# Optimization experiments

Measured on AMD Instinct MI355X. Metric: run time of the kernel, lower is better.

## Reference

```python
import jax, jax.numpy as jnp
import numpy as np

B, N, A = 8, 256, 180  # batch, resolution (even), n_angles


def setup_inputs() -> dict:
    key = jax.random.key(0)
    imgs = jax.random.normal(jax.random.fold_in(key, 0), (B, N, N), dtype=jnp.float32)
    # uniformly spaced projection angles over [0, pi)
    angles = jnp.linspace(0.0, np.pi, A, endpoint=False).astype(jnp.float32)
    return {"imgs": imgs, "angles": angles}


def _radon_forward(imgs, angles):
    """Parallel-beam Radon forward projection via bilinear ray sampling.

    imgs:   [B, N, N] float image batch
    angles: [A] float projection angles (radians)
    returns sinogram [B, A, N] (detector count == resolution, unit step along ray)
    """
    n = imgs.shape[-1]
    dtype = imgs.dtype
    c = (n - 1) / 2.0  # image center in pixel coords
    s = jnp.arange(n, dtype=dtype) - c  # detector positions, centered
    t = s                                # integration steps along each ray
    cos = jnp.cos(angles)[:, None, None]  # [A,1,1]
    sin = jnp.sin(angles)[:, None, None]
    # Sample point for (angle a, detector s_i, step t_j), in pixel coordinates.
    x = s[None, :, None] * cos - t[None, None, :] * sin + c  # [A, N, N]
    y = s[None, :, None] * sin + t[None, None, :] * cos + c  # [A, N, N]

    x0 = jnp.floor(x)
    y0 = jnp.floor(y)
    wx = x - x0
    wy = y - y0
    x0i = x0.astype(jnp.int32)
    y0i = y0.astype(jnp.int32)

    def corner(xi, yi, w):
        # zero-padding outside the image: mask out-of-range samples
        inb = (xi >= 0) & (xi < n) & (yi >= 0) & (yi < n)
        xc = jnp.clip(xi, 0, n - 1)
        yc = jnp.clip(yi, 0, n - 1)
        vals = imgs[:, yc, xc]  # gather -> [B, A, N, N]
        return vals * (w * inb.astype(dtype))[None]

    acc = (corner(x0i, y0i, (1.0 - wx) * (1.0 - wy))
           + corner(x0i + 1, y0i, wx * (1.0 - wy))
           + corner(x0i, y0i + 1, (1.0 - wx) * wy)
           + corner(x0i + 1, y0i + 1, wx * wy))
    return acc.sum(axis=-1)  # line integral along t -> [B, A, N]


def reference(imgs, angles):
    return _radon_forward(imgs, angles)
```

## Files before the change

kernel.cpp:

```cpp
#include <hip/hip_runtime.h>
#include <hip/hip_fp16.h>

#define NREZ 256
#define NB 8
#define NA 180

#define GW 258
#define GBYTES ((size_t)GW * GW * 16)

#define LWMAX 52
#define LH 47
#define CHUNK_T 32
#define NCHUNK (NREZ / CHUNK_T)

__device__ __forceinline__ __half2 bc_h2(unsigned int v) {
    return __builtin_bit_cast(__half2, v);
}

__device__ __forceinline__ void dma16(const uint4* g, uint4* l) {
    __builtin_amdgcn_global_load_lds(
        (const __attribute__((address_space(1))) void*)g,
        (__attribute__((address_space(3))) void*)l, 16, 0, 0);
}

__global__ __launch_bounds__(256) void build_fp16g(const float* __restrict__ img,
                                                   uint4* __restrict__ gbuf) {
    const int gy = blockIdx.x;
    for (int gx = threadIdx.x; gx < GW; gx += 256) {
        uint4 v = make_uint4(0u, 0u, 0u, 0u);
        const int x = gx - 1, y = gy - 1;
        if (x >= 0 && x < NREZ && y >= 0 && y < NREZ) {
            const int p = (y << 8) + x;
            unsigned short h[NB];
#pragma unroll
            for (int b = 0; b < NB; ++b)
                h[b] = __half_as_ushort(__float2half_rn(img[b * (NREZ * NREZ) + p]));
            v.x = (unsigned)h[0] | ((unsigned)h[1] << 16);
            v.y = (unsigned)h[2] | ((unsigned)h[3] << 16);
            v.z = (unsigned)h[4] | ((unsigned)h[5] << 16);
            v.w = (unsigned)h[6] | ((unsigned)h[7] << 16);
        }
        gbuf[(size_t)gy * GW + gx] = v;
    }
}

__global__ __launch_bounds__(256, 4) void radon_dma(const uint4* __restrict__ gbuf,
                                                    const float* __restrict__ angles,
                                                    float* __restrict__ out) {
    __shared__ uint4 tile[LWMAX * LH];

    const int a = blockIdx.x;
    const int tid = threadIdx.x;
    const int wave = tid >> 6;
    const int lane = tid & 63;
    const int ls = lane & 31;
    const int lp = lane >> 5;
    const int sIdx = blockIdx.y * 32 + ls;
    const int tw = 2 * wave + lp;

    const float C = 127.5f;
    float sn, cs;
    sincosf(angles[a], &sn, &cs);

    int LWr = 47;
    {
        float best = -1.f;
#pragma unroll
        for (int w = 47; w <= LWMAX; ++w) {
            const float sig = fmaf(sn, (float)w, cs);
            const float u = sig - 2.f * floorf(sig * 0.5f);
            const float m = 1.f - fabsf(u - 1.f);
            if (m > best) { best = m; LWr = w; }
        }
    }

    const float s = (float)sIdx - C;
    const float xs = fmaf(s, cs, C);
    const float ys = fmaf(s, sn, C);

    const float s_lo = (float)(blockIdx.y * 32) - C;
    const float s_hi = s_lo + 31.f;
    const float xsl = fmaf(s_lo, cs, C), xsh = fmaf(s_hi, cs, C);
    const float ysl = fmaf(s_lo, sn, C), ysh = fmaf(s_hi, sn, C);

    auto window = [&](int ck, int& bxs, int& bys, bool& interior, bool& empty,
                      int& hh, int& wl) {
        const float t_lo = (float)(ck * CHUNK_T) - C;
        const float t_hi = t_lo + 31.f;
        const float x00 = fmaf(t_lo, -sn, xsl), x01 = fmaf(t_hi, -sn, xsl);
        const float x10 = fmaf(t_lo, -sn, xsh), x11 = fmaf(t_hi, -sn, xsh);
        const float y00 = fmaf(t_lo, cs, ysl), y01 = fmaf(t_hi, cs, ysl);
        const float y10 = fmaf(t_lo, cs, ysh), y11 = fmaf(t_hi, cs, ysh);
        const int bx = (int)floorf(fminf(fminf(x00, x01), fminf(x10, x11)));
        const int by = (int)floorf(fminf(fminf(y00, y01), fminf(y10, y11)));
        const int mx = (int)floorf(fmaxf(fmaxf(x00, x01), fmaxf(x10, x11)));
        const int my = (int)floorf(fmaxf(fmaxf(y00, y01), fmaxf(y10, y11)));
        bxs = min(max(bx, -1), 210);
        bys = min(max(by, -1), 210);
        interior = (bx >= 0) && (by >= 0) && (bx <= 210) && (by <= 210);
        empty = (bx > 255) || (by > 255) || (mx < -1) || (my < -1);
        hh = min(LH, max(my - bys + 2, 0));
        wl = interior ? 46 : 47;
    };

    auto stage = [&](int bxs, int bys, int hh, int wl) {
#pragma unroll
        for (int k = 0; k < 12; ++k) {
            const int row = wave + 4 * k;
            if (row < hh && lane < wl) {
                const uint4* gp = gbuf + (size_t)(bys + row + 1) * GW + (bxs + 1) + lane;
                dma16(gp, &tile[row * LWr]);
            }
        }
    };

    float accf[NB];
#pragma unroll
    for (int b = 0; b < NB; ++b) accf[b] = 0.f;
    const __half2 hz = __float2half2_rn(0.f);

    int bxs, bys, hh, wl;
    bool interior, empty;
    window(0, bxs, bys, interior, empty, hh, wl);
    if (!empty) stage(bxs, bys, hh, wl);

    for (int ck = 0; ck < NCHUNK; ++ck) {
        __syncthreads();

        const float t_lo = (float)(ck * CHUNK_T) - C;
        __half2 acc01 = hz, acc23 = hz, acc45 = hz, acc67 = hz;

        auto samp = [&](float tt, bool chk) {
            const float x = fmaf(tt, -sn, xs);
            const float y = fmaf(tt, cs, ys);
            const float xf = floorf(x), yf = floorf(y);
            const int u0 = (int)xf, v0 = (int)yf;
            if (!chk || (u0 >= -1 && u0 <= 255 && v0 >= -1 && v0 <= 255)) {
                const float wu = x - xf, wv = y - yf;
                const float au = 1.f - wu, av = 1.f - wv;
                const __half2 w00 = __float2half2_rn(au * av);
                const __half2 w10 = __float2half2_rn(wu * av);
                const __half2 w01 = __float2half2_rn(au * wv);
                const __half2 w11 = __float2half2_rn(wu * wv);
                const int dx = u0 - bxs;
                const int r = v0 - bys;
                const int b00 = r * LWr + dx;
                const int b10 = b00 + LWr;
                const uint4 p00 = tile[b00];
                const uint4 p10 = tile[b00 + 1];
                const uint4 p01 = tile[b10];
                const uint4 p11 = tile[b10 + 1];
                acc01 = __hfma2(w00, bc_h2(p00.x), acc01);
                acc01 = __hfma2(w10, bc_h2(p10.x), acc01);
                acc01 = __hfma2(w01, bc_h2(p01.x), acc01);
                acc01 = __hfma2(w11, bc_h2(p11.x), acc01);
                acc23 = __hfma2(w00, bc_h2(p00.y), acc23);
                acc23 = __hfma2(w10, bc_h2(p10.y), acc23);
                acc23 = __hfma2(w01, bc_h2(p01.y), acc23);
                acc23 = __hfma2(w11, bc_h2(p11.y), acc23);
                acc45 = __hfma2(w00, bc_h2(p00.z), acc45);
                acc45 = __hfma2(w10, bc_h2(p10.z), acc45);
                acc45 = __hfma2(w01, bc_h2(p01.z), acc45);
                acc45 = __hfma2(w11, bc_h2(p11.z), acc45);
                acc67 = __hfma2(w00, bc_h2(p00.w), acc67);
                acc67 = __hfma2(w10, bc_h2(p10.w), acc67);
                acc67 = __hfma2(w01, bc_h2(p01.w), acc67);
                acc67 = __hfma2(w11, bc_h2(p11.w), acc67);
            }
        };

        if (!empty) {
            if (interior) {
#pragma unroll
                for (int it = 0; it < 4; ++it)
                    samp(t_lo + (float)(tw + 8 * it), false);
            } else {
#pragma unroll
                for (int it = 0; it < 4; ++it)
                    samp(t_lo + (float)(tw + 8 * it), true);
            }
            accf[0] += __low2float(acc01); accf[1] += __high2float(acc01);
            accf[2] += __low2float(acc23); accf[3] += __high2float(acc23);
            accf[4] += __low2float(acc45); accf[5] += __high2float(acc45);
            accf[6] += __low2float(acc67); accf[7] += __high2float(acc67);
        }

        __syncthreads();

        if (ck + 1 < NCHUNK) {
            window(ck + 1, bxs, bys, interior, empty, hh, wl);
            if (!empty) stage(bxs, bys, hh, wl);
        }
    }

#pragma unroll
    for (int b = 0; b < NB; ++b) accf[b] += __shfl_xor(accf[b], 32);

    float4* red4 = (float4*)tile;
    if (lane < 32) {
        red4[(wave * 32 + lane) * 2 + 0] = make_float4(accf[0], accf[1], accf[2], accf[3]);
        red4[(wave * 32 + lane) * 2 + 1] = make_float4(accf[4], accf[5], accf[6], accf[7]);
    }
    __syncthreads();
    {
        const float* red = (const float*)tile;
        const int b = tid >> 5;
        const int ss = tid & 31;
        const int base = ss * 8 + b;
        const float sum = red[base] + red[256 + base] + red[512 + base] + red[768 + base];
        out[(b * NA + a) * NREZ + blockIdx.y * 32 + ss] = sum;
    }
}

__global__ __launch_bounds__(256) void radon_plain(const float* __restrict__ img,
                                                   const float* __restrict__ angles,
                                                   float* __restrict__ out) {
    const int a = blockIdx.x;
    const int tid = threadIdx.x;
    const int wave = tid >> 6;
    const int lane = tid & 63;
    const int s_sub = lane & 7;
    const int t_sub = lane >> 3;
    const int sIdx = blockIdx.y * 32 + wave * 8 + s_sub;
    const float c = 127.5f;
    float sn, cs;
    sincosf(angles[a], &sn, &cs);
    const float s = (float)sIdx - c;
    float acc[NB];
#pragma unroll
    for (int b = 0; b < NB; ++b) acc[b] = 0.f;
    for (int j = 0; j < NREZ / 8; ++j) {
        const float tt = (float)(t_sub + 8 * j) - c;
        const float x = s * cs - tt * sn + c;
        const float y = s * sn + tt * cs + c;
        const float xf = floorf(x), yf = floorf(y);
        const int u0 = (int)xf, v0 = (int)yf;
        if (u0 < -1 || u0 >= NREZ || v0 < -1 || v0 >= NREZ) continue;
        const float wu = x - xf, wv = y - yf;
        const bool iu0 = (u0 >= 0), iu1 = (u0 + 1 <= NREZ - 1);
        const bool iv0 = (v0 >= 0), iv1 = (v0 + 1 <= NREZ - 1);
        const float w00 = (1.f - wu) * (1.f - wv) * ((iu0 && iv0) ? 1.f : 0.f);
        const float w10 = wu * (1.f - wv) * ((iu1 && iv0) ? 1.f : 0.f);
        const float w01 = (1.f - wu) * wv * ((iu0 && iv1) ? 1.f : 0.f);
        const float w11 = wu * wv * ((iu1 && iv1) ? 1.f : 0.f);
        const int u0c = min(max(u0, 0), NREZ - 1);
        const int u1c = min(u0 + 1, NREZ - 1);
        const int v0c = min(max(v0, 0), NREZ - 1);
        const int v1c = min(v0 + 1, NREZ - 1);
#pragma unroll
        for (int b = 0; b < NB; ++b) {
            const float* p = img + b * (NREZ * NREZ);
            acc[b] += w00 * p[v0c * NREZ + u0c] + w10 * p[v0c * NREZ + u1c] +
                      w01 * p[v1c * NREZ + u0c] + w11 * p[v1c * NREZ + u1c];
        }
    }
#pragma unroll
    for (int b = 0; b < NB; ++b) {
        float v = acc[b];
        v += __shfl_xor(v, 8);
        v += __shfl_xor(v, 16);
        v += __shfl_xor(v, 32);
        acc[b] = v;
    }
    if (t_sub == 0) {
#pragma unroll
        for (int b = 0; b < NB; ++b) out[(b * NA + a) * NREZ + sIdx] = acc[b];
    }
}

extern "C" void kernel_launch(void* const* d_in, const int* in_sizes, int n_in,
                              void* d_out, int out_size, void* d_ws, size_t ws_size,
                              hipStream_t stream) {
    (void)in_sizes; (void)n_in; (void)out_size;
    const float* imgs = (const float*)d_in[0];
    const float* angles = (const float*)d_in[1];
    float* out = (float*)d_out;

    dim3 grid(NA, NREZ / 32);
    if (ws_size >= GBYTES) {
        uint4* gbuf = (uint4*)d_ws;
        build_fp16g<<<GW, 256, 0, stream>>>(imgs, gbuf);
        radon_dma<<<grid, 256, 0, stream>>>(gbuf, angles, out);
    } else {
        radon_plain<<<grid, 256, 0, stream>>>(imgs, angles, out);
    }
}
```

Measured before the change: 92.78 us.

## Double-buffer LDS tiles and halve chunk length to overlap DMA with sampling

Splits the ray integration into 16-step chunks with smaller LDS windows and double-buffers them, so the global-to-LDS DMA for the next chunk is issued right after one barrier while the current chunk is sampled. This removes one barrier per chunk and hides staging latency behind the bilinear sampling work. The cost is twice as many chunks, more window and staging overhead per sample, a larger shared-memory footprint, and a lower launch-bounds occupancy hint (3 instead of 4).

```diff
diff --git a/kernel.cpp b/kernel.cpp
--- a/kernel.cpp
+++ b/kernel.cpp
@@ -8,9 +8,11 @@
 #define GW 258
 #define GBYTES ((size_t)GW * GW * 16)
 
-#define LWMAX 52
-#define LH 47
-#define CHUNK_T 32
+#define LH 37
+#define LWMIN 41
+#define LWMAX 43
+#define TSTRIDE (LWMAX * LH)
+#define CHUNK_T 16
 #define NCHUNK (NREZ / CHUNK_T)
 
 __device__ __forceinline__ __half2 bc_h2(unsigned int v) {
@@ -44,10 +46,10 @@
     }
 }
 
-__global__ __launch_bounds__(256, 4) void radon_dma(const uint4* __restrict__ gbuf,
+__global__ __launch_bounds__(256, 3) void radon_dma(const uint4* __restrict__ gbuf,
                                                     const float* __restrict__ angles,
                                                     float* __restrict__ out) {
-    __shared__ uint4 tile[LWMAX * LH];
+    __shared__ uint4 tile[2 * TSTRIDE];
 
     const int a = blockIdx.x;
     const int tid = threadIdx.x;
@@ -62,11 +64,11 @@
     float sn, cs;
     sincosf(angles[a], &sn, &cs);
 
-    int LWr = 47;
+    int LWr = LWMIN;
     {
         float best = -1.f;
 #pragma unroll
-        for (int w = 47; w <= LWMAX; ++w) {
+        for (int w = LWMIN; w <= LWMAX; ++w) {
             const float sig = fmaf(sn, (float)w, cs);
             const float u = sig - 2.f * floorf(sig * 0.5f);
             const float m = 1.f - fabsf(u - 1.f);
@@ -83,10 +85,9 @@
     const float xsl = fmaf(s_lo, cs, C), xsh = fmaf(s_hi, cs, C);
     const float ysl = fmaf(s_lo, sn, C), ysh = fmaf(s_hi, sn, C);
 
-    auto window = [&](int ck, int& bxs, int& bys, bool& interior, bool& empty,
-                      int& hh, int& wl) {
+    auto window = [&](int ck, int& bxs, int& bys, bool& interior, bool& empty, int& hh) {
         const float t_lo = (float)(ck * CHUNK_T) - C;
-        const float t_hi = t_lo + 31.f;
+        const float t_hi = t_lo + 15.f;
         const float x00 = fmaf(t_lo, -sn, xsl), x01 = fmaf(t_hi, -sn, xsl);
         const float x10 = fmaf(t_lo, -sn, xsh), x11 = fmaf(t_hi, -sn, xsh);
         const float y00 = fmaf(t_lo, cs, ysl), y01 = fmaf(t_hi, cs, ysl);
@@ -95,21 +96,20 @@
         const int by = (int)floorf(fminf(fminf(y00, y01), fminf(y10, y11)));
         const int mx = (int)floorf(fmaxf(fmaxf(x00, x01), fmaxf(x10, x11)));
         const int my = (int)floorf(fmaxf(fmaxf(y00, y01), fmaxf(y10, y11)));
-        bxs = min(max(bx, -1), 210);
-        bys = min(max(by, -1), 210);
-        interior = (bx >= 0) && (by >= 0) && (bx <= 210) && (by <= 210);
+        bxs = min(max(bx, -1), 220);
+        bys = min(max(by, -1), 220);
+        interior = (bx >= 0) && (by >= 0) && (bx <= 219) && (by <= 219);
         empty = (bx > 255) || (by > 255) || (mx < -1) || (my < -1);
         hh = min(LH, max(my - bys + 2, 0));
-        wl = interior ? 46 : 47;
     };
 
-    auto stage = [&](int bxs, int bys, int hh, int wl) {
-#pragma unroll
-        for (int k = 0; k < 12; ++k) {
+    auto stage = [&](uint4* dst, int bxs, int bys, int hh) {
+#pragma unroll
+        for (int k = 0; k < 10; ++k) {
             const int row = wave + 4 * k;
-            if (row < hh && lane < wl) {
+            if (row < hh && lane < 37) {
                 const uint4* gp = gbuf + (size_t)(bys + row + 1) * GW + (bxs + 1) + lane;
-                dma16(gp, &tile[row * LWr]);
+                dma16(gp, dst + row * LWr);
             }
         }
     };
@@ -119,77 +119,80 @@
     for (int b = 0; b < NB; ++b) accf[b] = 0.f;
     const __half2 hz = __float2half2_rn(0.f);
 
-    int bxs, bys, hh, wl;
-    bool interior, empty;
-    window(0, bxs, bys, interior, empty, hh, wl);
-    if (!empty) stage(bxs, bys, hh, wl);
+    int cbx, cby, chh, nbx, nby, nhh;
+    bool cint, cemp, nint, nemp;
+    window(0, cbx, cby, cint, cemp, chh);
+    if (!cemp) stage(tile, cbx, cby, chh);
 
     for (int ck = 0; ck < NCHUNK; ++ck) {
+        const bool haveNext = (ck + 1 < NCHUNK);
+        if (haveNext) window(ck + 1, nbx, nby, nint, nemp, nhh);
+
         __syncthreads();
 
-        const float t_lo = (float)(ck * CHUNK_T) - C;
-        __half2 acc01 = hz, acc23 = hz, acc45 = hz, acc67 = hz;
-
-        auto samp = [&](float tt, bool chk) {
-            const float x = fmaf(tt, -sn, xs);
-            const float y = fmaf(tt, cs, ys);
-            const float xf = floorf(x), yf = floorf(y);
-            const int u0 = (int)xf, v0 = (int)yf;
-            if (!chk || (u0 >= -1 && u0 <= 255 && v0 >= -1 && v0 <= 255)) {
-                const float wu = x - xf, wv = y - yf;
-                const float au = 1.f - wu, av = 1.f - wv;
-                const __half2 w00 = __float2half2_rn(au * av);
-                const __half2 w10 = __float2half2_rn(wu * av);
-                const __half2 w01 = __float2half2_rn(au * wv);
-                const __half2 w11 = __float2half2_rn(wu * wv);
-                const int dx = u0 - bxs;
-                const int r = v0 - bys;
-                const int b00 = r * LWr + dx;
-                const int b10 = b00 + LWr;
-                const uint4 p00 = tile[b00];
-                const uint4 p10 = tile[b00 + 1];
-                const uint4 p01 = tile[b10];
-                const uint4 p11 = tile[b10 + 1];
-                acc01 = __hfma2(w00, bc_h2(p00.x), acc01);
-                acc01 = __hfma2(w10, bc_h2(p10.x), acc01);
-                acc01 = __hfma2(w01, bc_h2(p01.x), acc01);
-                acc01 = __hfma2(w11, bc_h2(p11.x), acc01);
-                acc23 = __hfma2(w00, bc_h2(p00.y), acc23);
-                acc23 = __hfma2(w10, bc_h2(p10.y), acc23);
-                acc23 = __hfma2(w01, bc_h2(p01.y), acc23);
-                acc23 = __hfma2(w11, bc_h2(p11.y), acc23);
-                acc45 = __hfma2(w00, bc_h2(p00.z), acc45);
-                acc45 = __hfma2(w10, bc_h2(p10.z), acc45);
-                acc45 = __hfma2(w01, bc_h2(p01.z), acc45);
-                acc45 = __hfma2(w11, bc_h2(p11.z), acc45);
-                acc67 = __hfma2(w00, bc_h2(p00.w), acc67);
-                acc67 = __hfma2(w10, bc_h2(p10.w), acc67);
-                acc67 = __hfma2(w01, bc_h2(p01.w), acc67);
-                acc67 = __hfma2(w11, bc_h2(p11.w), acc67);
+        if (haveNext && !nemp)
+            stage(tile + ((ck + 1) & 1) * TSTRIDE, nbx, nby, nhh);
+
+        if (!cemp) {
+            const uint4* __restrict__ tl = tile + (ck & 1) * TSTRIDE;
+            const float t_lo = (float)(ck * CHUNK_T) - C;
+            __half2 acc01 = hz, acc23 = hz, acc45 = hz, acc67 = hz;
+
+            auto samp = [&](float tt, bool chk) {
+                const float x = fmaf(tt, -sn, xs);
+                const float y = fmaf(tt, cs, ys);
+                const float xf = floorf(x), yf = floorf(y);
+                const int u0 = (int)xf, v0 = (int)yf;
+                if (!chk || (u0 >= -1 && u0 <= 255 && v0 >= -1 && v0 <= 255)) {
+                    const float wu = x - xf, wv = y - yf;
+                    const float au = 1.f - wu, av = 1.f - wv;
+                    const __half2 w00 = __float2half2_rn(au * av);
+                    const __half2 w10 = __float2half2_rn(wu * av);
+                    const __half2 w01 = __float2half2_rn(au * wv);
+                    const __half2 w11 = __float2half2_rn(wu * wv);
+                    const int dx = u0 - cbx;
+                    const int r = v0 - cby;
+                    const int b00 = r * LWr + dx;
+                    const int b10 = b00 + LWr;
+                    const uint4 p00 = tl[b00];
+                    const uint4 p10 = tl[b00 + 1];
+                    const uint4 p01 = tl[b10];
+                    const uint4 p11 = tl[b10 + 1];
+                    acc01 = __hfma2(w00, bc_h2(p00.x), acc01);
+                    acc01 = __hfma2(w10, bc_h2(p10.x), acc01);
+                    acc01 = __hfma2(w01, bc_h2(p01.x), acc01);
+                    acc01 = __hfma2(w11, bc_h2(p11.x), acc01);
+                    acc23 = __hfma2(w00, bc_h2(p00.y), acc23);
+                    acc23 = __hfma2(w10, bc_h2(p10.y), acc23);
+                    acc23 = __hfma2(w01, bc_h2(p01.y), acc23);
+                    acc23 = __hfma2(w11, bc_h2(p11.y), acc23);
+                    acc45 = __hfma2(w00, bc_h2(p00.z), acc45);
+                    acc45 = __hfma2(w10, bc_h2(p10.z), acc45);
+                    acc45 = __hfma2(w01, bc_h2(p01.z), acc45);
+                    acc45 = __hfma2(w11, bc_h2(p11.z), acc45);
+                    acc67 = __hfma2(w00, bc_h2(p00.w), acc67);
+                    acc67 = __hfma2(w10, bc_h2(p10.w), acc67);
+                    acc67 = __hfma2(w01, bc_h2(p01.w), acc67);
+                    acc67 = __hfma2(w11, bc_h2(p11.w), acc67);
+                }
+            };
+
+            if (cint) {
+                samp(t_lo + (float)tw, false);
+                samp(t_lo + (float)(tw + 8), false);
+            } else {
+                samp(t_lo + (float)tw, true);
+                samp(t_lo + (float)(tw + 8), true);
             }
-        };
-
-        if (!empty) {
-            if (interior) {
-#pragma unroll
-                for (int it = 0; it < 4; ++it)
-                    samp(t_lo + (float)(tw + 8 * it), false);
-            } else {
-#pragma unroll
-                for (int it = 0; it < 4; ++it)
-                    samp(t_lo + (float)(tw + 8 * it), true);
-            }
+
             accf[0] += __low2float(acc01); accf[1] += __high2float(acc01);
             accf[2] += __low2float(acc23); accf[3] += __high2float(acc23);
             accf[4] += __low2float(acc45); accf[5] += __high2float(acc45);
             accf[6] += __low2float(acc67); accf[7] += __high2float(acc67);
         }
 
-        __syncthreads();
-
-        if (ck + 1 < NCHUNK) {
-            window(ck + 1, bxs, bys, interior, empty, hh, wl);
-            if (!empty) stage(bxs, bys, hh, wl);
+        if (haveNext) {
+            cbx = nbx; cby = nby; chh = nhh; cint = nint; cemp = nemp;
         }
     }
 
```

New measurement: 104.7 us. +12.8%, slower.
